# Kernel tuning notes

Measured on AMD Instinct MI355X. Metric: run time of the kernel, lower is better.

Reference implementation:

```python
import jax, jax.numpy as jnp
import numpy as np

D_MODEL = 256

def setup_inputs() -> dict:
    key = jax.random.key(0)
    k_x, k_wqkv, k_bqkv, k_wp, k_bp = jax.random.split(key, 5)
    B, T, d = 4, 4096, D_MODEL
    bound_qkv = 1.0 / np.sqrt(d)
    return {
        "x": jax.random.normal(k_x, (B, T, d), dtype=jnp.float32),
        "W_qkv": jax.random.uniform(k_wqkv, (d, 3 * d), jnp.float32, -bound_qkv, bound_qkv),
        "b_qkv": jax.random.uniform(k_bqkv, (3 * d,), jnp.float32, -bound_qkv, bound_qkv),
        "W_proj": jax.random.uniform(k_wp, (d, d), jnp.float32, -bound_qkv, bound_qkv),
        "b_proj": jax.random.uniform(k_bp, (d,), jnp.float32, -bound_qkv, bound_qkv),
    }

def reference(x, W_qkv, b_qkv, W_proj, b_proj):
    B, T, d = x.shape
    qkv = x @ W_qkv + b_qkv                       # (B, T, 3d)
    q, k, v = jnp.split(qkv, 3, axis=-1)          # each (B, T, d)
    scale = 1.0 / np.sqrt(d).astype(np.float32)
    scores = jnp.einsum('btd,bsd->bts', q, k) * scale   # (B, T, T)
    causal = jnp.tril(jnp.ones((T, T), dtype=bool))     # allowed positions
    scores = jnp.where(causal, scores, -jnp.inf)
    weights = jax.nn.softmax(scores, axis=-1)           # (B, T, T)
    ctx = jnp.einsum('bts,bsd->btd', weights, v)        # (B, T, d)
    return ctx @ W_proj + b_proj
```

## Files before the change

kernel.cpp:

```cpp
#include <hip/hip_runtime.h>
#include <math.h>

#define TT 4096
#define BB 4
#define DM 256
#define NSEG_B 144

typedef __attribute__((ext_vector_type(8))) short short8;
typedef __attribute__((ext_vector_type(4))) short short4v;
typedef __attribute__((ext_vector_type(4))) float f32x4;

#define MFMA16(a, b, c) __builtin_amdgcn_mfma_f32_16x16x32_bf16(a, b, c, 0, 0, 0)

#define GL2LDS(gp, lp) __builtin_amdgcn_global_load_lds( \
    (const __attribute__((address_space(1))) unsigned int*)(gp), \
    (__attribute__((address_space(3))) unsigned int*)(lp), 16, 0, 0)

__device__ __forceinline__ short f2b(float f) {
    union { float f; unsigned u; } v; v.f = f;
    unsigned r = v.u + 0x7FFFu + ((v.u >> 16) & 1u);
    return (short)(r >> 16);
}
__device__ __forceinline__ float b2f(short h) {
    union { unsigned u; float f; } v;
    v.u = ((unsigned)(unsigned short)h) << 16;
    return v.f;
}

__global__ __launch_bounds__(256) void transpose_cast2(
    const float* __restrict__ W1, short* __restrict__ Wt1,
    const float* __restrict__ W2, short* __restrict__ Wt2)
{
    __shared__ float T[64 * 68];
    const int tid = threadIdx.x;
    const int by = blockIdx.y;
    const float* W; short* Wt; int N, n0;
    if (by < 12) { W = W1; Wt = Wt1; N = 768; n0 = by * 64; }
    else         { W = W2; Wt = Wt2; N = 256; n0 = (by - 12) * 64; }
    const int k0 = blockIdx.x * 64;
#pragma unroll
    for (int it = 0; it < 4; ++it) {
        int idx = tid + it * 256;
        int r = idx >> 4, c4 = idx & 15;
        *(float4*)&T[r * 68 + c4 * 4] =
            *(const float4*)&W[(size_t)(k0 + r) * N + n0 + c4 * 4];
    }
    __syncthreads();
#pragma unroll
    for (int it = 0; it < 4; ++it) {
        int idx = tid + it * 256;
        int n = idx >> 4, c4 = idx & 15;
        short4v t;
#pragma unroll
        for (int j = 0; j < 4; ++j) t[j] = f2b(T[(c4 * 4 + j) * 68 + n]);
        *(short4v*)&Wt[(size_t)(n0 + n) * 256 + k0 + c4 * 4] = t;
    }
}

__global__ __launch_bounds__(256) void qkv_gemm(
    const float* __restrict__ x, const short* __restrict__ Bt,
    const float* __restrict__ bias, short* __restrict__ qkvb,
    short* __restrict__ VtG)
{
    __shared__ short As[16384];
    __shared__ short Bs[16384];
    __shared__ short Ts[64 * 72];

    const int tid = threadIdx.x;
    const int w = tid >> 6, lane = tid & 63;
    const int l15 = lane & 15, quad = lane >> 4;
    const int m0 = blockIdx.x * 64;
    const int nsup = blockIdx.y * 384;

#pragma unroll
    for (int it = 0; it < 8; ++it) {
        int idx = tid + it * 256;
        int row = ((idx >> 9) << 4) + (idx & 15);
        int col = ((idx >> 6) & 7) * 32 + ((idx >> 4) & 3) * 8;
        const float* src = &x[(size_t)(m0 + row) * 256 + col];
        float4 u = *(const float4*)src, u2 = *(const float4*)(src + 4);
        short8 t;
        t[0] = f2b(u.x);  t[1] = f2b(u.y);  t[2] = f2b(u.z);  t[3] = f2b(u.w);
        t[4] = f2b(u2.x); t[5] = f2b(u2.y); t[6] = f2b(u2.z); t[7] = f2b(u2.w);
        *(short8*)&As[idx * 8] = t;
    }

    for (int t6 = 0; t6 < 6; ++t6) {
        const int n0 = nsup + t6 * 64;
#pragma unroll
        for (int it = 0; it < 8; ++it) {
            int idx = tid + it * 256;
            int n = ((idx >> 9) << 4) + (idx & 15);
            int col = ((idx >> 6) & 7) * 32 + ((idx >> 4) & 3) * 8;
            *(short8*)&Bs[idx * 8] = *(const short8*)&Bt[(size_t)(n0 + n) * 256 + col];
        }
        __syncthreads();

        f32x4 acc[4];
#pragma unroll
        for (int t = 0; t < 4; ++t) acc[t] = (f32x4){0.f, 0.f, 0.f, 0.f};
#pragma unroll
        for (int k0 = 0; k0 < 8; ++k0) {
            short8 a = *(const short8*)&As[((w * 8 + k0) * 64 + lane) * 8];
#pragma unroll
            for (int nt = 0; nt < 4; ++nt) {
                short8 bb = *(const short8*)&Bs[((nt * 8 + k0) * 64 + lane) * 8];
                acc[nt] = MFMA16(a, bb, acc[nt]);
            }
        }

        if (n0 < 512) {
#pragma unroll
            for (int nt = 0; nt < 4; ++nt) {
                int n = n0 + nt * 16 + l15;
                float bv = bias[n];
#pragma unroll
                for (int r = 0; r < 4; ++r)
                    qkvb[(size_t)(m0 + w * 16 + quad * 4 + r) * 768 + n]
                        = f2b(acc[nt][r] + bv);
            }
            __syncthreads();
        } else {
#pragma unroll
            for (int nt = 0; nt < 4; ++nt) {
                int n = n0 + nt * 16 + l15;
                float bv = bias[n];
#pragma unroll
                for (int r = 0; r < 4; ++r)
                    Ts[(nt * 16 + l15) * 72 + w * 16 + quad * 4 + r]
                        = f2b(acc[nt][r] + bv);
            }
            __syncthreads();
            const int d  = tid >> 2;
            const int c  = tid & 3;
            short8 v0 = *(const short8*)&Ts[d * 72 + c * 16];
            short8 v1 = *(const short8*)&Ts[d * 72 + c * 16 + 8];
            const int bg = m0 >> 12, key0 = (m0 & 4095) + c * 16;
            short* dst = &VtG[((size_t)bg * 256 + (n0 - 512) + d) * 4096 + key0];
            *(short8*)dst = v0;
            *(short8*)(dst + 8) = v1;
        }
    }
}

__global__ __launch_bounds__(256, 2) void flash_mfma(
    const short* __restrict__ qkv,
    const short* __restrict__ VtG,
    short* __restrict__ Opart,
    float* __restrict__ L)
{
    __shared__ short Ks[2][4096];
    __shared__ short Vs[8192];
    __shared__ short Ps[4096];

    const int tid = threadIdx.x;
    const int w = tid >> 6, lane = tid & 63;
    const int l15 = lane & 15, quad = lane >> 4;

    const int b = blockIdx.x & 3;
    const int e = (NSEG_B - 1) - (blockIdx.x >> 2);
    const int lid = b * NSEG_B + e;
    int g = 0;
    while (g < 7 && e >= 2 * (g + 1) * (g + 2)) ++g;
    int off = e - 2 * g * (g + 1);
    int qt = 4 * g + off / (g + 1);
    int s  = off - (off / (g + 1)) * (g + 1);
    const int kp_lo = s * 16;
    const int kp_hi = min(kp_lo + 16, 4 * (qt + 1));
    const int npairs = kp_hi - kp_lo;

    const size_t base = (size_t)b * TT * 768;
    const int row0 = qt * 128;

    short8 aq[2][8];
#pragma unroll
    for (int rs = 0; rs < 2; ++rs) {
        const short* qrow = &qkv[base + (size_t)(row0 + rs * 64 + w * 16 + l15) * 768 + quad * 8];
#pragma unroll
        for (int k0 = 0; k0 < 8; ++k0)
            aq[rs][k0] = *(const short8*)&qrow[k0 * 32];
    }

#pragma unroll
    for (int it = 0; it < 2; ++it) {
        int idx = tid + it * 256;
        int row = idx & 15;
        int col = ((idx >> 6) & 7) * 32 + ((idx >> 4) & 3) * 8;
        GL2LDS(&qkv[base + (size_t)(kp_lo * 32 + row) * 768 + 256 + col], &Ks[0][idx * 8]);
    }

    f32x4 o[2][16];
#pragma unroll
    for (int rs = 0; rs < 2; ++rs)
#pragma unroll
        for (int c = 0; c < 16; ++c) o[rs][c] = (f32x4){0.f, 0.f, 0.f, 0.f};
    float l_acc[2][4] = {{0.f, 0.f, 0.f, 0.f}, {0.f, 0.f, 0.f, 0.f}};

    for (int u = 0; u < npairs; ++u) {
        const int j0 = (kp_lo + u) * 32;

        __syncthreads();

#pragma unroll
        for (int it = 0; it < 2; ++it) {
            int idx = tid + it * 256;
            int row = idx & 15;
            int col = ((idx >> 6) & 7) * 32 + ((idx >> 4) & 3) * 8;
            GL2LDS(&qkv[base + (size_t)(j0 + 16 + row) * 768 + 256 + col], &Ks[1][idx * 8]);
        }
        __builtin_amdgcn_sched_barrier(0);
#pragma unroll
        for (int it = 0; it < 4; ++it) {
            int idx = tid + it * 256;
            int d  = ((idx >> 6) << 4) + (idx & 15);
            int kc = ((idx >> 4) & 3) * 8;
            GL2LDS(&VtG[((size_t)b * 256 + d) * 4096 + j0 + kc], &Vs[idx * 8]);
        }
        __builtin_amdgcn_sched_barrier(0);

        {
            f32x4 s4[2];
            s4[0] = (f32x4){0.f, 0.f, 0.f, 0.f};
            s4[1] = (f32x4){0.f, 0.f, 0.f, 0.f};
#pragma unroll
            for (int k0 = 0; k0 < 8; ++k0) {
                short8 bb = *(const short8*)&Ks[0][(k0 * 64 + lane) * 8];
                s4[0] = MFMA16(aq[0][k0], bb, s4[0]);
                s4[1] = MFMA16(aq[1][k0], bb, s4[1]);
            }
#pragma unroll
            for (int rs = 0; rs < 2; ++rs)
#pragma unroll
                for (int r = 0; r < 4; ++r) {
                    const int rg = row0 + rs * 64 + w * 16 + quad * 4 + r;
                    int jg = j0 + l15;
                    float xx = s4[rs][r] * 0.0625f;
                    if (jg > rg) xx = -INFINITY;
                    float pv = __expf(fminf(xx, 30.f));
                    l_acc[rs][r] += pv;
                    Ps[((rs * 4 + w) * 64 + (0 * 2 + (l15 >> 3)) * 16 + quad * 4 + r) * 8
                       + (l15 & 7)] = f2b(pv);
                }
        }

        asm volatile("s_waitcnt vmcnt(4)" ::: "memory");
        __builtin_amdgcn_s_barrier();
        __builtin_amdgcn_sched_barrier(0);

        if (u + 1 < npairs) {
#pragma unroll
            for (int it = 0; it < 2; ++it) {
                int idx = tid + it * 256;
                int row = idx & 15;
                int col = ((idx >> 6) & 7) * 32 + ((idx >> 4) & 3) * 8;
                GL2LDS(&qkv[base + (size_t)(j0 + 32 + row) * 768 + 256 + col], &Ks[0][idx * 8]);
            }
        }
        __builtin_amdgcn_sched_barrier(0);

        {
            f32x4 s4[2];
            s4[0] = (f32x4){0.f, 0.f, 0.f, 0.f};
            s4[1] = (f32x4){0.f, 0.f, 0.f, 0.f};
#pragma unroll
            for (int k0 = 0; k0 < 8; ++k0) {
                short8 bb = *(const short8*)&Ks[1][(k0 * 64 + lane) * 8];
                s4[0] = MFMA16(aq[0][k0], bb, s4[0]);
                s4[1] = MFMA16(aq[1][k0], bb, s4[1]);
            }
#pragma unroll
            for (int rs = 0; rs < 2; ++rs)
#pragma unroll
                for (int r = 0; r < 4; ++r) {
                    const int rg = row0 + rs * 64 + w * 16 + quad * 4 + r;
                    int jg = j0 + 16 + l15;
                    float xx = s4[rs][r] * 0.0625f;
                    if (jg > rg) xx = -INFINITY;
                    float pv = __expf(fminf(xx, 30.f));
                    l_acc[rs][r] += pv;
                    Ps[((rs * 4 + w) * 64 + (1 * 2 + (l15 >> 3)) * 16 + quad * 4 + r) * 8
                       + (l15 & 7)] = f2b(pv);
                }
        }

        if (u + 1 < npairs) {
            asm volatile("s_waitcnt vmcnt(2)" ::: "memory");
        } else {
            asm volatile("s_waitcnt vmcnt(0)" ::: "memory");
        }
        __builtin_amdgcn_s_barrier();
        __builtin_amdgcn_sched_barrier(0);

        {
            short8 a0 = *(const short8*)&Ps[((0 * 4 + w) * 64 + lane) * 8];
            short8 a1 = *(const short8*)&Ps[((1 * 4 + w) * 64 + lane) * 8];
#pragma unroll
            for (int ct = 0; ct < 16; ++ct) {
                short8 bb = *(const short8*)&Vs[(ct * 64 + lane) * 8];
                o[0][ct] = MFMA16(a0, bb, o[0][ct]);
                o[1][ct] = MFMA16(a1, bb, o[1][ct]);
            }
        }
    }

#pragma unroll
    for (int rs = 0; rs < 2; ++rs)
#pragma unroll
        for (int r = 0; r < 4; ++r) {
            float l = l_acc[rs][r];
            l += __shfl_xor(l, 1); l += __shfl_xor(l, 2);
            l += __shfl_xor(l, 4); l += __shfl_xor(l, 8);
            if (l15 == 0)
                L[(size_t)lid * 128 + rs * 64 + w * 16 + quad * 4 + r] = l;
        }
    const size_t ob = (size_t)lid * (128 * 256);
#pragma unroll
    for (int rs = 0; rs < 2; ++rs)
#pragma unroll
        for (int r = 0; r < 4; ++r) {
            int lr = rs * 64 + w * 16 + quad * 4 + r;
#pragma unroll
            for (int c = 0; c < 16; ++c)
                Opart[ob + (size_t)lr * 256 + c * 16 + l15] = f2b(o[rs][c][r]);
        }
}

__global__ __launch_bounds__(256) void proj_gemm(
    const short* __restrict__ Opart, const float* __restrict__ L,
    const short* __restrict__ Bt, const float* __restrict__ bias,
    float* __restrict__ out)
{
    __shared__ short As[8192];
    __shared__ short Bs[16384];
    __shared__ float Linv[32];

    const int tid = threadIdx.x;
    const int w = tid >> 6, lane = tid & 63;
    const int l15 = lane & 15, quad = lane >> 4;
    const int t = blockIdx.x;
    const int b = t >> 7, q32 = t & 127;
    const int qt = q32 >> 2;
    const int ro = (q32 & 3) * 32;
    const int gg = qt >> 2, rr = qt & 3;
    const int sbase = b * NSEG_B + 2 * gg * (gg + 1) + rr * (gg + 1);
    const int nseg = gg + 1;
    const int m0 = t * 32;

    if (tid < 32) {
        float l = 0.f;
#pragma unroll
        for (int s2 = 0; s2 < 8; ++s2)
            if (s2 < nseg) l += L[(size_t)(sbase + s2) * 128 + ro + tid];
        Linv[tid] = 1.f / l;
    }
    __syncthreads();

#pragma unroll
    for (int it = 0; it < 4; ++it) {
        int idx = tid + it * 256;
        int row = ((idx >> 9) << 4) + (idx & 15);
        int col = ((idx >> 6) & 7) * 32 + ((idx >> 4) & 3) * 8;
        float a8[8] = {0.f, 0.f, 0.f, 0.f, 0.f, 0.f, 0.f, 0.f};
#pragma unroll
        for (int s2 = 0; s2 < 8; ++s2) {
            if (s2 < nseg) {
                short8 hv = *(const short8*)&Opart[(size_t)(sbase + s2) * 32768
                                                   + (size_t)(ro + row) * 256 + col];
#pragma unroll
                for (int j = 0; j < 8; ++j) a8[j] += b2f(hv[j]);
            }
        }
        float inv = Linv[row];
        short8 t8;
#pragma unroll
        for (int j = 0; j < 8; ++j) t8[j] = f2b(a8[j] * inv);
        *(short8*)&As[idx * 8] = t8;
    }

    for (int t2 = 0; t2 < 4; ++t2) {
        const int n0 = t2 * 64;
#pragma unroll
        for (int it = 0; it < 8; ++it) {
            int idx = tid + it * 256;
            int n = ((idx >> 9) << 4) + (idx & 15);
            int col = ((idx >> 6) & 7) * 32 + ((idx >> 4) & 3) * 8;
            *(short8*)&Bs[idx * 8] = *(const short8*)&Bt[(size_t)(n0 + n) * 256 + col];
        }
        __syncthreads();

        f32x4 acc[2];
        acc[0] = (f32x4){0.f, 0.f, 0.f, 0.f};
        acc[1] = (f32x4){0.f, 0.f, 0.f, 0.f};
#pragma unroll
        for (int k0 = 0; k0 < 8; ++k0) {
            short8 a = *(const short8*)&As[(((w & 1) * 8 + k0) * 64 + lane) * 8];
#pragma unroll
            for (int nt = 0; nt < 2; ++nt) {
                int n16 = (w >> 1) * 2 + nt;
                short8 bb = *(const short8*)&Bs[((n16 * 8 + k0) * 64 + lane) * 8];
                acc[nt] = MFMA16(a, bb, acc[nt]);
            }
        }
#pragma unroll
        for (int nt = 0; nt < 2; ++nt) {
            int n = n0 + ((w >> 1) * 2 + nt) * 16 + l15;
            float bv = bias[n];
#pragma unroll
            for (int r = 0; r < 4; ++r)
                out[(size_t)(m0 + (w & 1) * 16 + quad * 4 + r) * 256 + n] = acc[nt][r] + bv;
        }
        __syncthreads();
    }
}

extern "C" void kernel_launch(void* const* d_in, const int* in_sizes, int n_in,
                              void* d_out, int out_size, void* d_ws, size_t ws_size,
                              hipStream_t stream)
{
    const float* x     = (const float*)d_in[0];
    const float* Wqkv  = (const float*)d_in[1];
    const float* bqkv  = (const float*)d_in[2];
    const float* Wproj = (const float*)d_in[3];
    const float* bproj = (const float*)d_in[4];
    float* out = (float*)d_out;

    const size_t M = (size_t)BB * TT;
    short* qkv_b = (short*)d_ws;
    short* Wt1   = qkv_b + M * 768;
    short* Wt2   = Wt1 + (size_t)768 * 256;
    short* VtG   = Wt2 + (size_t)256 * 256;
    short* Opart = VtG + (size_t)BB * 256 * 4096;
    float* L     = (float*)(Opart + (size_t)BB * NSEG_B * 128 * 256);

    transpose_cast2<<<dim3(4, 16), dim3(256), 0, stream>>>(Wqkv, Wt1, Wproj, Wt2);
    qkv_gemm<<<dim3(256, 2), dim3(256), 0, stream>>>(x, Wt1, bqkv, qkv_b, VtG);
    flash_mfma<<<dim3(BB * NSEG_B), dim3(256), 0, stream>>>(qkv_b, VtG, Opart, L);
    proj_gemm<<<dim3(512), dim3(256), 0, stream>>>(Opart, L, Wt2, bproj, out);
}
```

Measured before the change: 207.3 us.

## Rebalance causal flash attention with fixed-size work chunks per block and 256-row tiles

```diff
diff --git a/kernel.cpp b/kernel.cpp
--- a/kernel.cpp
+++ b/kernel.cpp
@@ -4,7 +4,7 @@
 #define TT 4096
 #define BB 4
 #define DM 256
-#define NSEG_B 144
+#define NSLOT 320
 
 typedef __attribute__((ext_vector_type(8))) short short8;
 typedef __attribute__((ext_vector_type(4))) short short4v;
@@ -143,7 +143,7 @@
     }
 }
 
-__global__ __launch_bounds__(256, 2) void flash_mfma(
+__global__ __launch_bounds__(512, 2) void flash_mfma(
     const short* __restrict__ qkv,
     const short* __restrict__ VtG,
     short* __restrict__ Opart,
@@ -151,178 +151,179 @@
 {
     __shared__ short Ks[2][4096];
     __shared__ short Vs[8192];
-    __shared__ short Ps[4096];
+    __shared__ short Ps[8192];
 
     const int tid = threadIdx.x;
     const int w = tid >> 6, lane = tid & 63;
     const int l15 = lane & 15, quad = lane >> 4;
 
-    const int b = blockIdx.x & 3;
-    const int e = (NSEG_B - 1) - (blockIdx.x >> 2);
-    const int lid = b * NSEG_B + e;
-    int g = 0;
-    while (g < 7 && e >= 2 * (g + 1) * (g + 2)) ++g;
-    int off = e - 2 * g * (g + 1);
-    int qt = 4 * g + off / (g + 1);
-    int s  = off - (off / (g + 1)) * (g + 1);
-    const int kp_lo = s * 16;
-    const int kp_hi = min(kp_lo + 16, 4 * (qt + 1));
-    const int npairs = kp_hi - kp_lo;
-
-    const size_t base = (size_t)b * TT * 768;
-    const int row0 = qt * 128;
-
-    short8 aq[2][8];
-#pragma unroll
-    for (int rs = 0; rs < 2; ++rs) {
-        const short* qrow = &qkv[base + (size_t)(row0 + rs * 64 + w * 16 + l15) * 768 + quad * 8];
-#pragma unroll
-        for (int k0 = 0; k0 < 8; ++k0)
-            aq[rs][k0] = *(const short8*)&qrow[k0 * 32];
-    }
-
-#pragma unroll
-    for (int it = 0; it < 2; ++it) {
-        int idx = tid + it * 256;
-        int row = idx & 15;
-        int col = ((idx >> 6) & 7) * 32 + ((idx >> 4) & 3) * 8;
-        GL2LDS(&qkv[base + (size_t)(kp_lo * 32 + row) * 768 + 256 + col], &Ks[0][idx * 8]);
-    }
-
-    f32x4 o[2][16];
-#pragma unroll
-    for (int rs = 0; rs < 2; ++rs)
-#pragma unroll
-        for (int c = 0; c < 16; ++c) o[rs][c] = (f32x4){0.f, 0.f, 0.f, 0.f};
-    float l_acc[2][4] = {{0.f, 0.f, 0.f, 0.f}, {0.f, 0.f, 0.f, 0.f}};
-
-    for (int u = 0; u < npairs; ++u) {
-        const int j0 = (kp_lo + u) * 32;
-
-        __syncthreads();
-
-#pragma unroll
-        for (int it = 0; it < 2; ++it) {
-            int idx = tid + it * 256;
+    int u_g = blockIdx.x * 17;
+    const int u_end = u_g + 17;
+
+    while (u_g < u_end) {
+        const int b = u_g / 1088;
+        const int u_b = u_g - b * 1088;
+        int qt = 0;
+        while (qt < 15 && u_b >= 4 * (qt + 1) * (qt + 2)) ++qt;
+        const int p0 = u_b - 4 * qt * (qt + 1);
+        const int navail = 8 * (qt + 1) - p0;
+        const int nrem = u_end - u_g;
+        const int npairs = navail < nrem ? navail : nrem;
+        const int sid = blockIdx.x + b * 16 + qt;
+
+        const size_t base = (size_t)b * TT * 768;
+        const int row0 = qt * 256;
+        const int kp_lo = p0;
+
+        short8 aq[2][8];
+#pragma unroll
+        for (int rs = 0; rs < 2; ++rs) {
+            const short* qrow = &qkv[base + (size_t)(row0 + rs * 128 + w * 16 + l15) * 768 + quad * 8];
+#pragma unroll
+            for (int k0 = 0; k0 < 8; ++k0)
+                aq[rs][k0] = *(const short8*)&qrow[k0 * 32];
+        }
+
+        {
+            int idx = tid;
             int row = idx & 15;
             int col = ((idx >> 6) & 7) * 32 + ((idx >> 4) & 3) * 8;
-            GL2LDS(&qkv[base + (size_t)(j0 + 16 + row) * 768 + 256 + col], &Ks[1][idx * 8]);
-        }
-        __builtin_amdgcn_sched_barrier(0);
-#pragma unroll
-        for (int it = 0; it < 4; ++it) {
-            int idx = tid + it * 256;
-            int d  = ((idx >> 6) << 4) + (idx & 15);
-            int kc = ((idx >> 4) & 3) * 8;
-            GL2LDS(&VtG[((size_t)b * 256 + d) * 4096 + j0 + kc], &Vs[idx * 8]);
-        }
-        __builtin_amdgcn_sched_barrier(0);
-
-        {
-            f32x4 s4[2];
-            s4[0] = (f32x4){0.f, 0.f, 0.f, 0.f};
-            s4[1] = (f32x4){0.f, 0.f, 0.f, 0.f};
-#pragma unroll
-            for (int k0 = 0; k0 < 8; ++k0) {
-                short8 bb = *(const short8*)&Ks[0][(k0 * 64 + lane) * 8];
-                s4[0] = MFMA16(aq[0][k0], bb, s4[0]);
-                s4[1] = MFMA16(aq[1][k0], bb, s4[1]);
-            }
-#pragma unroll
-            for (int rs = 0; rs < 2; ++rs)
-#pragma unroll
-                for (int r = 0; r < 4; ++r) {
-                    const int rg = row0 + rs * 64 + w * 16 + quad * 4 + r;
-                    int jg = j0 + l15;
-                    float xx = s4[rs][r] * 0.0625f;
-                    if (jg > rg) xx = -INFINITY;
-                    float pv = __expf(fminf(xx, 30.f));
-                    l_acc[rs][r] += pv;
-                    Ps[((rs * 4 + w) * 64 + (0 * 2 + (l15 >> 3)) * 16 + quad * 4 + r) * 8
-                       + (l15 & 7)] = f2b(pv);
+            GL2LDS(&qkv[base + (size_t)(kp_lo * 32 + row) * 768 + 256 + col], &Ks[0][idx * 8]);
+        }
+
+        f32x4 o[2][16];
+#pragma unroll
+        for (int rs = 0; rs < 2; ++rs)
+#pragma unroll
+            for (int c = 0; c < 16; ++c) o[rs][c] = (f32x4){0.f, 0.f, 0.f, 0.f};
+        float l_acc[2][4] = {{0.f, 0.f, 0.f, 0.f}, {0.f, 0.f, 0.f, 0.f}};
+
+        for (int u = 0; u < npairs; ++u) {
+            const int j0 = (kp_lo + u) * 32;
+
+            __syncthreads();
+
+            {
+                int idx = tid;
+                int row = idx & 15;
+                int col = ((idx >> 6) & 7) * 32 + ((idx >> 4) & 3) * 8;
+                GL2LDS(&qkv[base + (size_t)(j0 + 16 + row) * 768 + 256 + col], &Ks[1][idx * 8]);
+            }
+            __builtin_amdgcn_sched_barrier(0);
+#pragma unroll
+            for (int it = 0; it < 2; ++it) {
+                int idx = tid + it * 512;
+                int d  = ((idx >> 6) << 4) + (idx & 15);
+                int kc = ((idx >> 4) & 3) * 8;
+                GL2LDS(&VtG[((size_t)b * 256 + d) * 4096 + j0 + kc], &Vs[idx * 8]);
+            }
+            __builtin_amdgcn_sched_barrier(0);
+
+            {
+                f32x4 s4[2];
+                s4[0] = (f32x4){0.f, 0.f, 0.f, 0.f};
+                s4[1] = (f32x4){0.f, 0.f, 0.f, 0.f};
+#pragma unroll
+                for (int k0 = 0; k0 < 8; ++k0) {
+                    short8 bb = *(const short8*)&Ks[0][(k0 * 64 + lane) * 8];
+                    s4[0] = MFMA16(aq[0][k0], bb, s4[0]);
+                    s4[1] = MFMA16(aq[1][k0], bb, s4[1]);
                 }
-        }
-
-        asm volatile("s_waitcnt vmcnt(4)" ::: "memory");
-        __builtin_amdgcn_s_barrier();
-        __builtin_amdgcn_sched_barrier(0);
-
-        if (u + 1 < npairs) {
-#pragma unroll
-            for (int it = 0; it < 2; ++it) {
-                int idx = tid + it * 256;
+#pragma unroll
+                for (int rs = 0; rs < 2; ++rs)
+#pragma unroll
+                    for (int r = 0; r < 4; ++r) {
+                        const int rg = row0 + rs * 128 + w * 16 + quad * 4 + r;
+                        int jg = j0 + l15;
+                        float xx = s4[rs][r] * 0.0625f;
+                        if (jg > rg) xx = -INFINITY;
+                        float pv = __expf(fminf(xx, 30.f));
+                        l_acc[rs][r] += pv;
+                        Ps[((rs * 8 + w) * 64 + (0 * 2 + (l15 >> 3)) * 16 + quad * 4 + r) * 8
+                           + (l15 & 7)] = f2b(pv);
+                    }
+            }
+
+            asm volatile("s_waitcnt vmcnt(2)" ::: "memory");
+            __builtin_amdgcn_s_barrier();
+            __builtin_amdgcn_sched_barrier(0);
+
+            if (u + 1 < npairs) {
+                int idx = tid;
                 int row = idx & 15;
                 int col = ((idx >> 6) & 7) * 32 + ((idx >> 4) & 3) * 8;
                 GL2LDS(&qkv[base + (size_t)(j0 + 32 + row) * 768 + 256 + col], &Ks[0][idx * 8]);
             }
-        }
-        __builtin_amdgcn_sched_barrier(0);
-
-        {
-            f32x4 s4[2];
-            s4[0] = (f32x4){0.f, 0.f, 0.f, 0.f};
-            s4[1] = (f32x4){0.f, 0.f, 0.f, 0.f};
-#pragma unroll
-            for (int k0 = 0; k0 < 8; ++k0) {
-                short8 bb = *(const short8*)&Ks[1][(k0 * 64 + lane) * 8];
-                s4[0] = MFMA16(aq[0][k0], bb, s4[0]);
-                s4[1] = MFMA16(aq[1][k0], bb, s4[1]);
-            }
-#pragma unroll
-            for (int rs = 0; rs < 2; ++rs)
-#pragma unroll
-                for (int r = 0; r < 4; ++r) {
-                    const int rg = row0 + rs * 64 + w * 16 + quad * 4 + r;
-                    int jg = j0 + 16 + l15;
-                    float xx = s4[rs][r] * 0.0625f;
-                    if (jg > rg) xx = -INFINITY;
-                    float pv = __expf(fminf(xx, 30.f));
-                    l_acc[rs][r] += pv;
-                    Ps[((rs * 4 + w) * 64 + (1 * 2 + (l15 >> 3)) * 16 + quad * 4 + r) * 8
-                       + (l15 & 7)] = f2b(pv);
+            __builtin_amdgcn_sched_barrier(0);
+
+            {
+                f32x4 s4[2];
+                s4[0] = (f32x4){0.f, 0.f, 0.f, 0.f};
+                s4[1] = (f32x4){0.f, 0.f, 0.f, 0.f};
+#pragma unroll
+                for (int k0 = 0; k0 < 8; ++k0) {
+                    short8 bb = *(const short8*)&Ks[1][(k0 * 64 + lane) * 8];
+                    s4[0] = MFMA16(aq[0][k0], bb, s4[0]);
+                    s4[1] = MFMA16(aq[1][k0], bb, s4[1]);
                 }
-        }
-
-        if (u + 1 < npairs) {
-            asm volatile("s_waitcnt vmcnt(2)" ::: "memory");
-        } else {
-            asm volatile("s_waitcnt vmcnt(0)" ::: "memory");
-        }
-        __builtin_amdgcn_s_barrier();
-        __builtin_amdgcn_sched_barrier(0);
-
-        {
-            short8 a0 = *(const short8*)&Ps[((0 * 4 + w) * 64 + lane) * 8];
-            short8 a1 = *(const short8*)&Ps[((1 * 4 + w) * 64 + lane) * 8];
-#pragma unroll
-            for (int ct = 0; ct < 16; ++ct) {
-                short8 bb = *(const short8*)&Vs[(ct * 64 + lane) * 8];
-                o[0][ct] = MFMA16(a0, bb, o[0][ct]);
-                o[1][ct] = MFMA16(a1, bb, o[1][ct]);
-            }
-        }
-    }
-
-#pragma unroll
-    for (int rs = 0; rs < 2; ++rs)
-#pragma unroll
-        for (int r = 0; r < 4; ++r) {
-            float l = l_acc[rs][r];
-            l += __shfl_xor(l, 1); l += __shfl_xor(l, 2);
-            l += __shfl_xor(l, 4); l += __shfl_xor(l, 8);
-            if (l15 == 0)
-                L[(size_t)lid * 128 + rs * 64 + w * 16 + quad * 4 + r] = l;
-        }
-    const size_t ob = (size_t)lid * (128 * 256);
-#pragma unroll
-    for (int rs = 0; rs < 2; ++rs)
-#pragma unroll
-        for (int r = 0; r < 4; ++r) {
-            int lr = rs * 64 + w * 16 + quad * 4 + r;
-#pragma unroll
-            for (int c = 0; c < 16; ++c)
-                Opart[ob + (size_t)lr * 256 + c * 16 + l15] = f2b(o[rs][c][r]);
-        }
+#pragma unroll
+                for (int rs = 0; rs < 2; ++rs)
+#pragma unroll
+                    for (int r = 0; r < 4; ++r) {
+                        const int rg = row0 + rs * 128 + w * 16 + quad * 4 + r;
+                        int jg = j0 + 16 + l15;
+                        float xx = s4[rs][r] * 0.0625f;
+                        if (jg > rg) xx = -INFINITY;
+                        float pv = __expf(fminf(xx, 30.f));
+                        l_acc[rs][r] += pv;
+                        Ps[((rs * 8 + w) * 64 + (1 * 2 + (l15 >> 3)) * 16 + quad * 4 + r) * 8
+                           + (l15 & 7)] = f2b(pv);
+                    }
+            }
+
+            if (u + 1 < npairs) {
+                asm volatile("s_waitcnt vmcnt(1)" ::: "memory");
+            } else {
+                asm volatile("s_waitcnt vmcnt(0)" ::: "memory");
+            }
+            __builtin_amdgcn_s_barrier();
+            __builtin_amdgcn_sched_barrier(0);
+
+            {
+                short8 a0 = *(const short8*)&Ps[((0 * 8 + w) * 64 + lane) * 8];
+                short8 a1 = *(const short8*)&Ps[((1 * 8 + w) * 64 + lane) * 8];
+#pragma unroll
+                for (int ct = 0; ct < 16; ++ct) {
+                    short8 bb = *(const short8*)&Vs[(ct * 64 + lane) * 8];
+                    o[0][ct] = MFMA16(a0, bb, o[0][ct]);
+                    o[1][ct] = MFMA16(a1, bb, o[1][ct]);
+                }
+            }
+        }
+
+#pragma unroll
+        for (int rs = 0; rs < 2; ++rs)
+#pragma unroll
+            for (int r = 0; r < 4; ++r) {
+                float l = l_acc[rs][r];
+                l += __shfl_xor(l, 1); l += __shfl_xor(l, 2);
+                l += __shfl_xor(l, 4); l += __shfl_xor(l, 8);
+                if (l15 == 0)
+                    L[(size_t)sid * 256 + rs * 128 + w * 16 + quad * 4 + r] = l;
+            }
+        const size_t ob = (size_t)sid * (256 * 256);
+#pragma unroll
+        for (int rs = 0; rs < 2; ++rs)
+#pragma unroll
+            for (int r = 0; r < 4; ++r) {
+                int lr = rs * 128 + w * 16 + quad * 4 + r;
+#pragma unroll
+                for (int c = 0; c < 16; ++c)
+                    Opart[ob + (size_t)lr * 256 + c * 16 + l15] = f2b(o[rs][c][r]);
+            }
+
+        u_g += npairs;
+    }
 }
 
 __global__ __launch_bounds__(256) void proj_gemm(
@@ -339,18 +340,22 @@
     const int l15 = lane & 15, quad = lane >> 4;
     const int t = blockIdx.x;
     const int b = t >> 7, q32 = t & 127;
-    const int qt = q32 >> 2;
-    const int ro = (q32 & 3) * 32;
-    const int gg = qt >> 2, rr = qt & 3;
-    const int sbase = b * NSEG_B + 2 * gg * (gg + 1) + rr * (gg + 1);
-    const int nseg = gg + 1;
+    const int qt = q32 >> 3;
+    const int ro = (q32 & 7) * 32;
+    const int T_glob = b * 16 + qt;
+    const int S = b * 1088 + 4 * qt * (qt + 1);
+    const int E = S + 8 * (qt + 1);
+    const int k_first = S / 17;
+    const int k_last = (E - 1) / 17;
+    const int nseg = k_last - k_first + 1;
+    const int sbase = k_first + T_glob;
     const int m0 = t * 32;
 
     if (tid < 32) {
         float l = 0.f;
 #pragma unroll
-        for (int s2 = 0; s2 < 8; ++s2)
-            if (s2 < nseg) l += L[(size_t)(sbase + s2) * 128 + ro + tid];
+        for (int s2 = 0; s2 < 9; ++s2)
+            if (s2 < nseg) l += L[(size_t)(sbase + s2) * 256 + ro + tid];
         Linv[tid] = 1.f / l;
     }
     __syncthreads();
@@ -362,9 +367,9 @@
         int col = ((idx >> 6) & 7) * 32 + ((idx >> 4) & 3) * 8;
         float a8[8] = {0.f, 0.f, 0.f, 0.f, 0.f, 0.f, 0.f, 0.f};
 #pragma unroll
-        for (int s2 = 0; s2 < 8; ++s2) {
+        for (int s2 = 0; s2 < 9; ++s2) {
             if (s2 < nseg) {
-                short8 hv = *(const short8*)&Opart[(size_t)(sbase + s2) * 32768
+                short8 hv = *(const short8*)&Opart[(size_t)(sbase + s2) * 65536
                                                    + (size_t)(ro + row) * 256 + col];
 #pragma unroll
                 for (int j = 0; j < 8; ++j) a8[j] += b2f(hv[j]);
@@ -430,10 +435,10 @@
     short* Wt2   = Wt1 + (size_t)768 * 256;
     short* VtG   = Wt2 + (size_t)256 * 256;
     short* Opart = VtG + (size_t)BB * 256 * 4096;
-    float* L     = (float*)(Opart + (size_t)BB * NSEG_B * 128 * 256);
+    float* L     = (float*)(Opart + (size_t)NSLOT * 256 * 256);
 
     transpose_cast2<<<dim3(4, 16), dim3(256), 0, stream>>>(Wqkv, Wt1, Wproj, Wt2);
     qkv_gemm<<<dim3(256, 2), dim3(256), 0, stream>>>(x, Wt1, bqkv, qkv_b, VtG);
-    flash_mfma<<<dim3(BB * NSEG_B), dim3(256), 0, stream>>>(qkv_b, VtG, Opart, L);
+    flash_mfma<<<dim3(256), dim3(512), 0, stream>>>(qkv_b, VtG, Opart, L);
     proj_gemm<<<dim3(512), dim3(256), 0, stream>>>(Opart, L, Wt2, bproj, out);
 }
```

Result: faster. 193.4 us (-6.7%).
